# Performance work log

Hardware: AMD Instinct MI355X
Metric: run time of the kernel (lower is better)

The kernel has to match this reference:

```python
import jax, jax.numpy as jnp
import numpy as np

B, S, D, H = 2, 2048, 1024, 16
HD = D // H  # head_dim = 64
SCALE = HD ** -0.5


def setup_inputs() -> dict:
    key = jax.random.key(0)
    k1, k2, k3 = jax.random.split(key, 3)
    src = jax.random.normal(k1, (B, S, D), dtype=jnp.float32)
    w_qkv = jax.random.normal(k2, (D, 3 * D), dtype=jnp.float32) * (D ** -0.5)
    b_qkv = jax.random.normal(k3, (3 * D,), dtype=jnp.float32) * 0.02
    return {"src": src, "w_qkv": w_qkv, "b_qkv": b_qkv}


def reference(src, w_qkv, b_qkv):
    # qkv projection: [B,S,3D]
    qkv = src @ w_qkv + b_qkv
    q, k, v = jnp.split(qkv, 3, axis=-1)
    # [B,S,D] -> [B,H,S,HD]
    def heads(x):
        return x.reshape(B, S, H, HD).transpose(0, 2, 1, 3)
    q, k, v = heads(q), heads(k), heads(v)
    # scaled dot-product attention (note: original scales AFTER q@k.T)
    attn = jnp.einsum('bhqd,bhkd->bhqk', q, k) * SCALE
    attn = jax.nn.softmax(attn, axis=-1)
    out = jnp.einsum('bhqk,bhkd->bhqd', attn, v)  # [B,H,S,HD]
    return out.transpose(0, 2, 1, 3).reshape(B, S, D)
```

## Files before the change

### kernel.cpp

```cpp
#include <hip/hip_runtime.h>
#include <hip/hip_bf16.h>

typedef short short8 __attribute__((ext_vector_type(8)));
typedef float f32x4 __attribute__((ext_vector_type(4)));
typedef float f32x16 __attribute__((ext_vector_type(16)));
typedef __hip_bfloat16 bf16;


__device__ __forceinline__ void glds16(const void* g, void* l) {
  __builtin_amdgcn_global_load_lds((const __attribute__((address_space(1))) unsigned int*)g,
                                   (__attribute__((address_space(3))) unsigned int*)l, 16, 0, 0);
}

__device__ __forceinline__ uint pk2(float a, float b) {
  union { bf16 h2[2]; uint u; } pk;
  pk.h2[0] = __float2bfloat16(a);
  pk.h2[1] = __float2bfloat16(b);
  return pk.u;
}

__global__ __launch_bounds__(256) void prep_kernel(const float4* __restrict__ in,
                                                   bf16* __restrict__ src_bf,
                                                   const float* __restrict__ w,
                                                   bf16* __restrict__ wt) {
  __shared__ float tile[32][33];
  const int bid = blockIdx.x;
  if (bid < 4096) {
    int i = bid * 256 + threadIdx.x;
    float4 v = in[i];
    union { bf16 h[4]; uint2 u; } pk;
    pk.h[0] = __float2bfloat16(v.x);
    pk.h[1] = __float2bfloat16(v.y);
    pk.h[2] = __float2bfloat16(v.z);
    pk.h[3] = __float2bfloat16(v.w);
    *(uint2*)(src_bf + (size_t)i * 4) = pk.u;
  } else {
    int id = bid - 4096;
    int x0 = (id % 96) * 32;
    int y0 = (id / 96) * 32;
    int tx = threadIdx.x & 31, ty = threadIdx.x >> 5;
#pragma unroll
    for (int i = 0; i < 4; i++) {
      int y = ty + i * 8;
      tile[y][tx] = w[(size_t)(y0 + y) * 3072 + x0 + tx];
    }
    __syncthreads();
#pragma unroll
    for (int i = 0; i < 4; i++) {
      int y = ty + i * 8;
      wt[(size_t)(x0 + y) * 1024 + y0 + tx] = __float2bfloat16(tile[tx][y]);
    }
  }
}

__global__ __launch_bounds__(256) void qkv_gemm_kernel(
    const bf16* __restrict__ A, const bf16* __restrict__ Bt,
    const float* __restrict__ bias,
    bf16* __restrict__ q_ws, bf16* __restrict__ k_ws, bf16* __restrict__ vt_ws) {
  __shared__ alignas(16) char AB[32768];
  const int tid = threadIdx.x;
  const int lane = tid & 63, wid = tid >> 6;
  const int lr = lane & 15, lg = lane >> 4;
  const int wm = wid >> 1, wn = wid & 1;
  const int m0 = blockIdx.x * 128, n0 = blockIdx.y * 128;

  const f32x4 z4 = {0.f, 0.f, 0.f, 0.f};
  f32x4 acc[4][4];
#pragma unroll
  for (int m = 0; m < 4; m++)
#pragma unroll
    for (int n = 0; n < 4; n++) acc[m][n] = z4;

  const int srow = lane >> 3;
  const int sseg = (lane & 7) ^ srow;
  const char* Ag = (const char*)A + (size_t)(m0 + wid * 32 + srow) * 2048 + sseg * 16;
  const char* Bg = (const char*)Bt + (size_t)(n0 + wid * 32 + srow) * 2048 + sseg * 16;
  char* Al = AB + wid * 4096;
  char* Bl = AB + 16384 + wid * 4096;
  const int xora = (lr & 7) << 4;

  for (int kt = 0; kt < 16; kt++) {
    __syncthreads();
#pragma unroll
    for (int c = 0; c < 4; c++) {
      glds16(Ag + (size_t)kt * 128 + c * 16384, Al + c * 1024);
      glds16(Bg + (size_t)kt * 128 + c * 16384, Bl + c * 1024);
    }
    asm volatile("s_waitcnt vmcnt(0)" ::: "memory");
    __syncthreads();
#pragma unroll
    for (int g = 0; g < 2; g++) {
      short8 af[4], bfr[4];
#pragma unroll
      for (int m = 0; m < 4; m++)
        af[m] = *(const short8*)(AB + (wm * 64 + m * 16 + lr) * 128 +
                                 ((g * 64 + lg * 16) ^ xora));
#pragma unroll
      for (int n = 0; n < 4; n++)
        bfr[n] = *(const short8*)(AB + 16384 + (wn * 64 + n * 16 + lr) * 128 +
                                  ((g * 64 + lg * 16) ^ xora));
#pragma unroll
      for (int m = 0; m < 4; m++)
#pragma unroll
        for (int n = 0; n < 4; n++)
          acc[m][n] = __builtin_amdgcn_mfma_f32_16x16x32_bf16(af[m], bfr[n], acc[m][n], 0, 0, 0);
    }
  }

  const int which = n0 >> 10;
  const float scl = (which == 0) ? 0.18033688f : 1.0f;
#pragma unroll
  for (int m = 0; m < 4; m++) {
    int row = m0 + wm * 64 + m * 16 + lg * 4;
    int b = row >> 11;
    int ss0 = row & 2047;
#pragma unroll
    for (int n = 0; n < 4; n++) {
      int col = n0 + wn * 64 + n * 16 + lr;
      int d = col & 1023;
      int h = d >> 6, hd = d & 63;
      size_t bh = (size_t)(b * 16 + h);
      float bv = bias[col];
      if (which == 2) {
        union { bf16 h4[4]; uint2 u; } pk;
#pragma unroll
        for (int r = 0; r < 4; r++) pk.h4[r] = __float2bfloat16(acc[m][n][r] + bv);
        *(uint2*)&vt_ws[(bh * 64 + hd) * 2048 + ss0] = pk.u;
      } else {
        bf16* dst = (which == 0) ? q_ws : k_ws;
#pragma unroll
        for (int r = 0; r < 4; r++)
          dst[(bh * 2048 + (ss0 + r)) * 64 + hd] = __float2bfloat16((acc[m][n][r] + bv) * scl);
      }
    }
  }
}

#define KPERM(p) (((p) & ~31) | ((p) & 3) | ((((p) >> 2) & 1) << 3) | \
                  ((((p) >> 3) & 1) << 4) | ((((p) >> 4) & 1) << 2))

__global__ __launch_bounds__(512) void attn7_kernel(
    const bf16* __restrict__ q_ws, const bf16* __restrict__ k_ws,
    const bf16* __restrict__ vt_ws, float* __restrict__ out) {
  __shared__ alignas(16) char smem[65536];
  const int tid = threadIdx.x;
  const int lane = tid & 63, wid = tid >> 6;
  const int lq = lane & 31, hi = lane >> 5;
  const int hi16 = hi * 16;
  const int xorv = (lq & 7) << 4;

  const int f = blockIdx.x;
  const int bh = (f & 7) * 4 + ((f >> 3) & 3);
  const int qb = f >> 5;
  const int b = bh >> 4, h = bh & 15;
  const int q0 = qb * 256 + wid * 32;

  short8 qf[4];
  {
    const bf16* qrow = q_ws + ((size_t)bh * 2048 + q0 + lq) * 64;
#pragma unroll
    for (int s = 0; s < 4; s++) qf[s] = *(const short8*)(qrow + s * 16 + hi * 8);
  }

  const int l8 = lane >> 3;
  const int segk = (lane & 7) ^ l8;
  const int p0 = wid * 16 + l8;
  const int p1 = p0 + 8;
  const char* kgl0 = (const char*)k_ws + (size_t)bh * 262144 +
                     (size_t)KPERM(p0) * 128 + segk * 16;
  const char* kgl1 = (const char*)k_ws + (size_t)bh * 262144 +
                     (size_t)KPERM(p1) * 128 + segk * 16;
  const int l16 = lane >> 4;
  const int d0v = (wid * 2 + 0) * 4 + l16;
  const int d1v = (wid * 2 + 1) * 4 + l16;
  const char* vg0 = (const char*)vt_ws + (size_t)bh * 262144 + (size_t)d0v * 4096 +
                    (((lane & 15) ^ (d0v & 15)) << 4);
  const char* vg1 = (const char*)vt_ws + (size_t)bh * 262144 + (size_t)d1v * 4096 +
                    (((lane & 15) ^ (d1v & 15)) << 4);

  f32x16 o0a, o0b, o1a, o1b, lacc;
#pragma unroll
  for (int r = 0; r < 16; r++) {
    o0a[r] = 0.f; o0b[r] = 0.f; o1a[r] = 0.f; o1b[r] = 0.f; lacc[r] = 0.f;
  }

  glds16(kgl0, smem + wid * 2048);
  glds16(kgl1, smem + wid * 2048 + 1024);
  glds16(vg0, smem + 32768 + wid * 2048);
  glds16(vg1, smem + 32768 + wid * 2048 + 1024);
  asm volatile("s_waitcnt vmcnt(0)" ::: "memory");
  __builtin_amdgcn_s_barrier();

  for (int kt = 0; kt < 16; ++kt) {
    const int kb_off = (kt & 1) * 16384;
    const int vb_off = 32768 + (kt & 1) * 16384;
    if (kt + 1 < 16) {
      const int nb = ((kt + 1) & 1) * 16384;
      glds16(kgl0 + (size_t)(kt + 1) * 16384, smem + nb + wid * 2048);
      glds16(kgl1 + (size_t)(kt + 1) * 16384, smem + nb + wid * 2048 + 1024);
      glds16(vg0 + (size_t)(kt + 1) * 256, smem + 32768 + nb + wid * 2048);
      glds16(vg1 + (size_t)(kt + 1) * 256, smem + 32768 + nb + wid * 2048 + 1024);
    }

    f32x16 s0, s1, s2, s3;
#pragma unroll
    for (int r = 0; r < 16; r++) { s0[r] = 0.f; s1[r] = 0.f; s2[r] = 0.f; s3[r] = 0.f; }
#pragma unroll
    for (int st = 0; st < 4; st++) {
      const int doff = (st * 32 + hi16) ^ xorv;
      short8 ka = *(const short8*)(smem + kb_off + lq * 128 + doff);
      short8 kb = *(const short8*)(smem + kb_off + (lq + 32) * 128 + doff);
      short8 kc = *(const short8*)(smem + kb_off + (lq + 64) * 128 + doff);
      short8 kd = *(const short8*)(smem + kb_off + (lq + 96) * 128 + doff);
      __builtin_amdgcn_s_setprio(1);
      s0 = __builtin_amdgcn_mfma_f32_32x32x16_bf16(ka, qf[st], s0, 0, 0, 0);
      s1 = __builtin_amdgcn_mfma_f32_32x32x16_bf16(kb, qf[st], s1, 0, 0, 0);
      s2 = __builtin_amdgcn_mfma_f32_32x32x16_bf16(kc, qf[st], s2, 0, 0, 0);
      s3 = __builtin_amdgcn_mfma_f32_32x32x16_bf16(kd, qf[st], s3, 0, 0, 0);
      __builtin_amdgcn_s_setprio(0);
    }

#pragma unroll
    for (int r = 0; r < 16; r++) {
      s0[r] = __builtin_amdgcn_exp2f(s0[r]);
      s1[r] = __builtin_amdgcn_exp2f(s1[r]);
      s2[r] = __builtin_amdgcn_exp2f(s2[r]);
      s3[r] = __builtin_amdgcn_exp2f(s3[r]);
    }
#pragma unroll
    for (int r = 0; r < 16; r++)
      lacc[r] += (s0[r] + s1[r]) + (s2[r] + s3[r]);

#define PV_KB(S, KB, OA, OB)                                                     \
  {                                                                              \
    union { uint u[4]; short8 s8; } ua, ub;                                      \
    ua.u[0] = pk2(S[0], S[1]);   ua.u[1] = pk2(S[2], S[3]);                      \
    ua.u[2] = pk2(S[8], S[9]);   ua.u[3] = pk2(S[10], S[11]);                    \
    ub.u[0] = pk2(S[4], S[5]);   ub.u[1] = pk2(S[6], S[7]);                      \
    ub.u[2] = pk2(S[12], S[13]); ub.u[3] = pk2(S[14], S[15]);                    \
    const int c0 = (((KB) * 4 + hi) ^ (lq & 15)) << 4;                           \
    const int c1 = (((KB) * 4 + 2 + hi) ^ (lq & 15)) << 4;                       \
    short8 va0 = *(const short8*)(smem + vb_off + lq * 256 + c0);                \
    short8 va1 = *(const short8*)(smem + vb_off + (lq + 32) * 256 + c0);         \
    short8 vb0 = *(const short8*)(smem + vb_off + lq * 256 + c1);                \
    short8 vb1 = *(const short8*)(smem + vb_off + (lq + 32) * 256 + c1);         \
    __builtin_amdgcn_s_setprio(1);                                               \
    OA = __builtin_amdgcn_mfma_f32_32x32x16_bf16(va0, ua.s8, OA, 0, 0, 0);       \
    OB = __builtin_amdgcn_mfma_f32_32x32x16_bf16(va1, ua.s8, OB, 0, 0, 0);       \
    OA = __builtin_amdgcn_mfma_f32_32x32x16_bf16(vb0, ub.s8, OA, 0, 0, 0);       \
    OB = __builtin_amdgcn_mfma_f32_32x32x16_bf16(vb1, ub.s8, OB, 0, 0, 0);       \
    __builtin_amdgcn_s_setprio(0);                                               \
  }
    PV_KB(s0, 0, o0a, o1a)
    PV_KB(s1, 1, o0b, o1b)
    PV_KB(s2, 2, o0a, o1a)
    PV_KB(s3, 3, o0b, o1b)
#undef PV_KB

    if (kt < 15) {
      asm volatile("s_waitcnt vmcnt(0)" ::: "memory");
      __builtin_amdgcn_s_barrier();
    }
  }
  __syncthreads();

  float l;
  {
    float sm[8];
#pragma unroll
    for (int i = 0; i < 8; i++) sm[i] = lacc[i] + lacc[i + 8];
#pragma unroll
    for (int i = 0; i < 4; i++) sm[i] += sm[i + 4];
    l = (sm[0] + sm[1]) + (sm[2] + sm[3]);
    l += __shfl_xor(l, 32);
  }
  f32x16 o0, o1;
#pragma unroll
  for (int r = 0; r < 16; r++) { o0[r] = o0a[r] + o0b[r]; o1[r] = o1a[r] + o1b[r]; }
  float* ep = (float*)(smem) + wid * 1024;
  const float invl = 1.f / l;
  const int eq = lane >> 1, eds = lane & 1;
  float* obase = out + ((size_t)b * 2048 + qb * 256 + wid * 32 + eq) * 1024 +
                 h * 64 + eds * 16;
#pragma unroll
  for (int db = 0; db < 2; db++) {
#pragma unroll
    for (int r = 0; r < 16; r++) {
      int d = (r & 3) + 8 * (r >> 2) + 4 * hi;
      float v = (db ? o1[r] : o0[r]) * invl;
      ep[lq * 32 + ((d + lq) & 31)] = v;
    }
#pragma unroll
    for (int c = 0; c < 4; c++) {
      float4 t;
      t.x = ep[eq * 32 + ((eds * 16 + 4 * c + 0 + eq) & 31)];
      t.y = ep[eq * 32 + ((eds * 16 + 4 * c + 1 + eq) & 31)];
      t.z = ep[eq * 32 + ((eds * 16 + 4 * c + 2 + eq) & 31)];
      t.w = ep[eq * 32 + ((eds * 16 + 4 * c + 3 + eq) & 31)];
      *(float4*)(obase + db * 32 + 4 * c) = t;
    }
  }
}

extern "C" void kernel_launch(void* const* d_in, const int* in_sizes, int n_in,
                              void* d_out, int out_size, void* d_ws, size_t ws_size,
                              hipStream_t stream) {
  (void)in_sizes; (void)n_in; (void)out_size; (void)ws_size;
  const float* src  = (const float*)d_in[0];
  const float* w    = (const float*)d_in[1];
  const float* bias = (const float*)d_in[2];
  float* out = (float*)d_out;

  char* ws = (char*)d_ws;
  bf16* src_bf = (bf16*)ws;
  bf16* wt_bf  = (bf16*)(ws + 8388608);
  bf16* q_ws   = (bf16*)(ws + 8388608 + 6291456);
  bf16* k_ws   = q_ws + 4194304;
  bf16* vt_ws  = k_ws + 4194304;

  prep_kernel<<<7168, 256, 0, stream>>>((const float4*)src, src_bf, w, wt_bf);
  qkv_gemm_kernel<<<dim3(32, 24), 256, 0, stream>>>(src_bf, wt_bf, bias, q_ws, k_ws, vt_ws);
  attn7_kernel<<<256, 512, 0, stream>>>(q_ws, k_ws, vt_ws, out);
}
```

Measured before the change: 90.22 us.

## Split attention blocks to 4 waves with 128 queries, doubling grid size

The attention kernel now uses 256-thread blocks, each covering 128 query rows instead of 256, and the grid doubles to 512 blocks. Each wave now issues four K and four V async LDS loads per tile instead of two, so the same 32KB K/V tiles are filled by fewer threads. More blocks should spread better across the CUs, at the cost of loading each K/V tile twice as often per query and using 64KB of LDS per smaller block. The blockIdx-to-(bh, qb) mapping is unchanged, so qb now ranges 0..15 over 128-row chunks.

```diff
diff --git a/kernel.cpp b/kernel.cpp
--- a/kernel.cpp
+++ b/kernel.cpp
@@ -139,7 +139,7 @@
 #define KPERM(p) (((p) & ~31) | ((p) & 3) | ((((p) >> 2) & 1) << 3) | \
                   ((((p) >> 3) & 1) << 4) | ((((p) >> 4) & 1) << 2))
 
-__global__ __launch_bounds__(512) void attn7_kernel(
+__global__ __launch_bounds__(256) void attn8_kernel(
     const bf16* __restrict__ q_ws, const bf16* __restrict__ k_ws,
     const bf16* __restrict__ vt_ws, float* __restrict__ out) {
   __shared__ alignas(16) char smem[65536];
@@ -153,7 +153,7 @@
   const int bh = (f & 7) * 4 + ((f >> 3) & 3);
   const int qb = f >> 5;
   const int b = bh >> 4, h = bh & 15;
-  const int q0 = qb * 256 + wid * 32;
+  const int q0 = qb * 128 + wid * 32;
 
   short8 qf[4];
   {
@@ -164,19 +164,17 @@
 
   const int l8 = lane >> 3;
   const int segk = (lane & 7) ^ l8;
-  const int p0 = wid * 16 + l8;
-  const int p1 = p0 + 8;
-  const char* kgl0 = (const char*)k_ws + (size_t)bh * 262144 +
-                     (size_t)KPERM(p0) * 128 + segk * 16;
-  const char* kgl1 = (const char*)k_ws + (size_t)bh * 262144 +
-                     (size_t)KPERM(p1) * 128 + segk * 16;
   const int l16 = lane >> 4;
-  const int d0v = (wid * 2 + 0) * 4 + l16;
-  const int d1v = (wid * 2 + 1) * 4 + l16;
-  const char* vg0 = (const char*)vt_ws + (size_t)bh * 262144 + (size_t)d0v * 4096 +
-                    (((lane & 15) ^ (d0v & 15)) << 4);
-  const char* vg1 = (const char*)vt_ws + (size_t)bh * 262144 + (size_t)d1v * 4096 +
-                    (((lane & 15) ^ (d1v & 15)) << 4);
+  const char* kgl[4];
+  const char* vgl[4];
+#pragma unroll
+  for (int c = 0; c < 4; c++) {
+    const int p = wid * 32 + c * 8 + l8;
+    kgl[c] = (const char*)k_ws + (size_t)bh * 262144 + (size_t)KPERM(p) * 128 + segk * 16;
+    const int dv = wid * 16 + c * 4 + l16;
+    vgl[c] = (const char*)vt_ws + (size_t)bh * 262144 + (size_t)dv * 4096 +
+             (((lane & 15) ^ (dv & 15)) << 4);
+  }
 
   f32x16 o0a, o0b, o1a, o1b, lacc;
 #pragma unroll
@@ -184,10 +182,11 @@
     o0a[r] = 0.f; o0b[r] = 0.f; o1a[r] = 0.f; o1b[r] = 0.f; lacc[r] = 0.f;
   }
 
-  glds16(kgl0, smem + wid * 2048);
-  glds16(kgl1, smem + wid * 2048 + 1024);
-  glds16(vg0, smem + 32768 + wid * 2048);
-  glds16(vg1, smem + 32768 + wid * 2048 + 1024);
+#pragma unroll
+  for (int c = 0; c < 4; c++) {
+    glds16(kgl[c], smem + wid * 4096 + c * 1024);
+    glds16(vgl[c], smem + 32768 + wid * 4096 + c * 1024);
+  }
   asm volatile("s_waitcnt vmcnt(0)" ::: "memory");
   __builtin_amdgcn_s_barrier();
 
@@ -196,10 +195,11 @@
     const int vb_off = 32768 + (kt & 1) * 16384;
     if (kt + 1 < 16) {
       const int nb = ((kt + 1) & 1) * 16384;
-      glds16(kgl0 + (size_t)(kt + 1) * 16384, smem + nb + wid * 2048);
-      glds16(kgl1 + (size_t)(kt + 1) * 16384, smem + nb + wid * 2048 + 1024);
-      glds16(vg0 + (size_t)(kt + 1) * 256, smem + 32768 + nb + wid * 2048);
-      glds16(vg1 + (size_t)(kt + 1) * 256, smem + 32768 + nb + wid * 2048 + 1024);
+#pragma unroll
+      for (int c = 0; c < 4; c++) {
+        glds16(kgl[c] + (size_t)(kt + 1) * 16384, smem + nb + wid * 4096 + c * 1024);
+        glds16(vgl[c] + (size_t)(kt + 1) * 256, smem + 32768 + nb + wid * 4096 + c * 1024);
+      }
     }
 
     f32x16 s0, s1, s2, s3;
@@ -280,7 +280,7 @@
   float* ep = (float*)(smem) + wid * 1024;
   const float invl = 1.f / l;
   const int eq = lane >> 1, eds = lane & 1;
-  float* obase = out + ((size_t)b * 2048 + qb * 256 + wid * 32 + eq) * 1024 +
+  float* obase = out + ((size_t)b * 2048 + qb * 128 + wid * 32 + eq) * 1024 +
                  h * 64 + eds * 16;
 #pragma unroll
   for (int db = 0; db < 2; db++) {
@@ -320,5 +320,5 @@
 
   prep_kernel<<<7168, 256, 0, stream>>>((const float4*)src, src_bf, w, wt_bf);
   qkv_gemm_kernel<<<dim3(32, 24), 256, 0, stream>>>(src_bf, wt_bf, bias, q_ws, k_ws, vt_ws);
-  attn7_kernel<<<256, 512, 0, stream>>>(q_ws, k_ws, vt_ws, out);
-}
+  attn8_kernel<<<512, 256, 0, stream>>>(q_ws, k_ws, vt_ws, out);
+}
```

Measured after the change: 108.1 us. +19.8%, slower.

## Deepen attention K/V pipeline, swizzle GEMM blocks by XCD, widen weight transpose

Applied to the files above, without the earlier changes.

The attention kernel goes from a double buffer to a quad buffer for K/V tiles in LDS (128KB). Loads are issued two tiles ahead, and the wait-plus-barrier runs every other iteration instead of every iteration. This is meant to hide global-to-LDS latency and cut synchronisation, at the cost of much more LDS per block. The QKV GEMM remaps block IDs so each XCD works on neighbouring M tiles, which should improve L2 reuse. The weight transpose in the prep kernel now handles 64x32 tiles and writes packed bf16 pairs, which cuts the block count and the number of store instructions.

```diff
diff --git a/kernel.cpp b/kernel.cpp
--- a/kernel.cpp
+++ b/kernel.cpp
@@ -23,7 +23,7 @@
                                                    bf16* __restrict__ src_bf,
                                                    const float* __restrict__ w,
                                                    bf16* __restrict__ wt) {
-  __shared__ float tile[32][33];
+  __shared__ float tile[64][33];
   const int bid = blockIdx.x;
   if (bid < 4096) {
     int i = bid * 256 + threadIdx.x;
@@ -37,18 +37,19 @@
   } else {
     int id = bid - 4096;
     int x0 = (id % 96) * 32;
-    int y0 = (id / 96) * 32;
+    int y0 = (id / 96) * 64;
     int tx = threadIdx.x & 31, ty = threadIdx.x >> 5;
 #pragma unroll
-    for (int i = 0; i < 4; i++) {
+    for (int i = 0; i < 8; i++) {
       int y = ty + i * 8;
       tile[y][tx] = w[(size_t)(y0 + y) * 3072 + x0 + tx];
     }
     __syncthreads();
 #pragma unroll
-    for (int i = 0; i < 4; i++) {
-      int y = ty + i * 8;
-      wt[(size_t)(x0 + y) * 1024 + y0 + tx] = __float2bfloat16(tile[tx][y]);
+    for (int j = 0; j < 4; j++) {
+      int r = ty + j * 8;
+      uint u = pk2(tile[2 * tx][r], tile[2 * tx + 1][r]);
+      *(uint*)&wt[(size_t)(x0 + r) * 1024 + y0 + 2 * tx] = u;
     }
   }
 }
@@ -62,7 +63,11 @@
   const int lane = tid & 63, wid = tid >> 6;
   const int lr = lane & 15, lg = lane >> 4;
   const int wm = wid >> 1, wn = wid & 1;
-  const int m0 = blockIdx.x * 128, n0 = blockIdx.y * 128;
+  const int lin = blockIdx.y * 32 + blockIdx.x;
+  const int xcd = lin & 7, idx = lin >> 3;
+  const int bx = xcd * 4 + (idx & 3);
+  const int by = idx >> 2;
+  const int m0 = bx * 128, n0 = by * 128;
 
   const f32x4 z4 = {0.f, 0.f, 0.f, 0.f};
   f32x4 acc[4][4];
@@ -139,10 +144,10 @@
 #define KPERM(p) (((p) & ~31) | ((p) & 3) | ((((p) >> 2) & 1) << 3) | \
                   ((((p) >> 3) & 1) << 4) | ((((p) >> 4) & 1) << 2))
 
-__global__ __launch_bounds__(512) void attn7_kernel(
+__global__ __launch_bounds__(512) void attn9_kernel(
     const bf16* __restrict__ q_ws, const bf16* __restrict__ k_ws,
     const bf16* __restrict__ vt_ws, float* __restrict__ out) {
-  __shared__ alignas(16) char smem[65536];
+  __shared__ alignas(16) char smem[131072];
   const int tid = threadIdx.x;
   const int lane = tid & 63, wid = tid >> 6;
   const int lq = lane & 31, hi = lane >> 5;
@@ -184,22 +189,25 @@
     o0a[r] = 0.f; o0b[r] = 0.f; o1a[r] = 0.f; o1b[r] = 0.f; lacc[r] = 0.f;
   }
 
-  glds16(kgl0, smem + wid * 2048);
-  glds16(kgl1, smem + wid * 2048 + 1024);
-  glds16(vg0, smem + 32768 + wid * 2048);
-  glds16(vg1, smem + 32768 + wid * 2048 + 1024);
+#pragma unroll
+  for (int p = 0; p < 2; p++) {
+    glds16(kgl0 + (size_t)p * 16384, smem + p * 16384 + wid * 2048);
+    glds16(kgl1 + (size_t)p * 16384, smem + p * 16384 + wid * 2048 + 1024);
+    glds16(vg0 + (size_t)p * 256, smem + 65536 + p * 16384 + wid * 2048);
+    glds16(vg1 + (size_t)p * 256, smem + 65536 + p * 16384 + wid * 2048 + 1024);
+  }
   asm volatile("s_waitcnt vmcnt(0)" ::: "memory");
   __builtin_amdgcn_s_barrier();
 
   for (int kt = 0; kt < 16; ++kt) {
-    const int kb_off = (kt & 1) * 16384;
-    const int vb_off = 32768 + (kt & 1) * 16384;
-    if (kt + 1 < 16) {
-      const int nb = ((kt + 1) & 1) * 16384;
-      glds16(kgl0 + (size_t)(kt + 1) * 16384, smem + nb + wid * 2048);
-      glds16(kgl1 + (size_t)(kt + 1) * 16384, smem + nb + wid * 2048 + 1024);
-      glds16(vg0 + (size_t)(kt + 1) * 256, smem + 32768 + nb + wid * 2048);
-      glds16(vg1 + (size_t)(kt + 1) * 256, smem + 32768 + nb + wid * 2048 + 1024);
+    const int kb_off = (kt & 3) * 16384;
+    const int vb_off = 65536 + (kt & 3) * 16384;
+    if (kt + 2 < 16) {
+      const int nb = ((kt + 2) & 3) * 16384;
+      glds16(kgl0 + (size_t)(kt + 2) * 16384, smem + nb + wid * 2048);
+      glds16(kgl1 + (size_t)(kt + 2) * 16384, smem + nb + wid * 2048 + 1024);
+      glds16(vg0 + (size_t)(kt + 2) * 256, smem + 65536 + nb + wid * 2048);
+      glds16(vg1 + (size_t)(kt + 2) * 256, smem + 65536 + nb + wid * 2048 + 1024);
     }
 
     f32x16 s0, s1, s2, s3;
@@ -257,7 +265,7 @@
     PV_KB(s3, 3, o0b, o1b)
 #undef PV_KB
 
-    if (kt < 15) {
+    if ((kt & 1) && kt < 15) {
       asm volatile("s_waitcnt vmcnt(0)" ::: "memory");
       __builtin_amdgcn_s_barrier();
     }
@@ -318,7 +326,7 @@
   bf16* k_ws   = q_ws + 4194304;
   bf16* vt_ws  = k_ws + 4194304;
 
-  prep_kernel<<<7168, 256, 0, stream>>>((const float4*)src, src_bf, w, wt_bf);
+  prep_kernel<<<5632, 256, 0, stream>>>((const float4*)src, src_bf, w, wt_bf);
   qkv_gemm_kernel<<<dim3(32, 24), 256, 0, stream>>>(src_bf, wt_bf, bias, q_ws, k_ws, vt_ws);
-  attn7_kernel<<<256, 512, 0, stream>>>(q_ws, k_ws, vt_ws, out);
-}
+  attn9_kernel<<<256, 512, 0, stream>>>(q_ws, k_ws, vt_ws, out);
+}
```

Result: no change. 89.74 us, median of 3 (-0.5%).
